# Kernel tuning notes

Measured on AMD Instinct MI355X. Metric: run time of the kernel, lower is better.

The kernel has to match this reference:

```python
import jax, jax.numpy as jnp
import numpy as np

N_NODES = 100000
N_EDGES = 1600000
IN_CH = 128
HID = 128   # 2 * out_channels
OUT = 64


def setup_inputs() -> dict:
    key = jax.random.key(0)
    ks = jax.random.split(key, 6)
    x = jax.random.normal(ks[0], (N_NODES, IN_CH), dtype=jnp.float32)
    edge_index = jax.random.randint(ks[1], (2, N_EDGES), 0, N_NODES, dtype=jnp.int64)
    # Glorot-ish scaled weights
    W1 = jax.random.normal(ks[2], (IN_CH, HID), dtype=jnp.float32) * (1.0 / np.sqrt(IN_CH))
    b1 = jnp.zeros((HID,), dtype=jnp.float32)
    Wmu = jax.random.normal(ks[3], (HID, OUT), dtype=jnp.float32) * (1.0 / np.sqrt(HID))
    bmu = jnp.zeros((OUT,), dtype=jnp.float32)
    Wlv = jax.random.normal(ks[4], (HID, OUT), dtype=jnp.float32) * (1.0 / np.sqrt(HID))
    blv = jnp.zeros((OUT,), dtype=jnp.float32)
    return {"x": x, "edge_index": edge_index, "W1": W1, "b1": b1,
            "Wmu": Wmu, "bmu": bmu, "Wlv": Wlv, "blv": blv}


def reference(x, edge_index, W1, b1, Wmu, bmu, Wlv, blv):
    n = x.shape[0]
    loops = jnp.arange(n, dtype=edge_index.dtype)
    src = jnp.concatenate([edge_index[0], loops])  # [E + N]
    dst = jnp.concatenate([edge_index[1], loops])
    # GCN symmetric normalization with self-loops (cached=True -> compute once, reuse)
    deg = jax.ops.segment_sum(jnp.ones_like(src, dtype=x.dtype), dst, num_segments=n)
    dinv = jnp.where(deg > 0, jax.lax.rsqrt(jnp.maximum(deg, 1.0)), 0.0)
    norm = (dinv[src] * dinv[dst])[:, None]  # [E+N, 1]

    def gcn(h, W, b):
        h = h @ W                              # dense transform first (smaller gather width)
        msg = h[src] * norm                    # gather + edge scaling
        return jax.ops.segment_sum(msg, dst, num_segments=n) + b

    h = jax.nn.relu(gcn(x, W1, b1))
    mu = gcn(h, Wmu, bmu)
    logvar = gcn(h, Wlv, blv)
    return (mu, logvar)
```

## Files before the change

### kernel.cpp

```cpp
#include <hip/hip_runtime.h>
#include <hip/hip_fp16.h>


using half8 = __attribute__((ext_vector_type(8))) _Float16;
using f32x4 = __attribute__((ext_vector_type(4))) float;
using f32x2 = __attribute__((ext_vector_type(2))) float;

constexpr int CAP = 8192;

__global__ void detect_kernel(const int* __restrict__ ei, int* __restrict__ mode,
                              int* __restrict__ bcnt, int K) {
    int lane = threadIdx.x & 63;
    for (int i = lane; i < K; i += 64) bcnt[i] = 0;
    int any = 0;
    for (int k = lane; k < 1024; k += 64) any |= ei[2 * k + 1];
    unsigned long long b = __ballot(any != 0);
    if (threadIdx.x == 0) *mode = (b == 0ull) ? 1 : 0;
}

__global__ __launch_bounds__(256) void partition_kernel(
    const int* __restrict__ ei, int E, int n, const int* __restrict__ mode,
    int* __restrict__ bcnt, unsigned* __restrict__ pairs) {
    __shared__ int hist[512];
    __shared__ int base[512];
    int t = threadIdx.x;
    for (int i = t; i < 512; i += 256) hist[i] = 0;
    __syncthreads();
    int m = *mode;
    int e0 = blockIdx.x * 8192;
    int s_[32], d_[32], o_[32];
#pragma unroll
    for (int k = 0; k < 32; ++k) {
        int e = e0 + k * 256 + t;
        d_[k] = -1;
        if (e < E) {
            int s = m ? ei[2 * e] : ei[e];
            int d = m ? ei[2 * (E + e)] : ei[E + e];
            if ((unsigned)d < (unsigned)n && (unsigned)s < (unsigned)n) {
                s_[k] = s;
                d_[k] = d;
                o_[k] = atomicAdd(&hist[d >> 8], 1);
            }
        }
    }
    __syncthreads();
    int K = (n + 255) >> 8;
    for (int b = t; b < K; b += 256) {
        int h = hist[b];
        base[b] = h ? atomicAdd(&bcnt[b], h) : 0;
    }
    __syncthreads();
#pragma unroll
    for (int k = 0; k < 32; ++k) {
        if (d_[k] >= 0) {
            int b = d_[k] >> 8;
            unsigned p = (unsigned)s_[k] | ((unsigned)(d_[k] & 255) << 24);
            pairs[(size_t)b * CAP + base[b] + o_[k]] = p;
        }
    }
}

__global__ __launch_bounds__(256) void build_kernel(
    const unsigned* __restrict__ pairs, const int* __restrict__ bcnt,
    int2* __restrict__ rowbe, float* __restrict__ dinv,
    int* __restrict__ csr_src, int n) {
    __shared__ int hist[256];
    __shared__ int wtot[4];
    int b = blockIdx.x;
    int cnt = bcnt[b];
    size_t gbase = (size_t)b * CAP;
    int tid = threadIdx.x, lane = tid & 63, wv = tid >> 6;
    hist[tid] = 0;
    __syncthreads();
    for (int i = tid; i < cnt; i += 256)
        atomicAdd(&hist[pairs[gbase + i] >> 24], 1);
    __syncthreads();
    int v = hist[tid];
    int incl = v;
#pragma unroll
    for (int off = 1; off < 64; off <<= 1) {
        int t = __shfl_up(incl, off, 64);
        if (lane >= off) incl += t;
    }
    if (lane == 63) wtot[wv] = incl;
    __syncthreads();
    int wo = 0;
    for (int w = 0; w < wv; ++w) wo += wtot[w];
    int ex = wo + incl - v;
    int node = (b << 8) + tid;
    if (node < n) {
        int beg = (int)gbase + ex;
        rowbe[node] = make_int2(beg, beg + v);
        dinv[node] = rsqrtf((float)(v + 1));
    }
    __syncthreads();
    hist[tid] = ex;
    __syncthreads();
    for (int i = tid; i < cnt; i += 256) {
        unsigned p = pairs[gbase + i];
        int pos = atomicAdd(&hist[p >> 24], 1);
        csr_src[gbase + pos] = (int)(p & 0x00FFFFFFu);
    }
}

template <int MODE>
__global__ __launch_bounds__(256) void agg_row_kernel(
    const __half* __restrict__ T, const float* __restrict__ dinv,
    const int2* __restrict__ rowbe, const int* __restrict__ csr_src,
    const float* __restrict__ biasa, const float* __restrict__ biasb,
    void* __restrict__ outa, void* __restrict__ outb, int n) {
    int wave = (int)((blockIdx.x * blockDim.x + threadIdx.x) >> 6);
    int lane = threadIdx.x & 63;
    if (wave >= n) return;
    const __half2* x2 = (const __half2*)T;
    float di = dinv[wave];
    float2 xf = __half22float2(x2[((size_t)wave << 6) + lane]);
    float ax = 0.f, ay = 0.f;
    int2 be = rowbe[wave];
    int e = be.x, end = be.y;
    for (; e + 8 <= end; e += 8) {
        int s[8];
        float w[8];
        float2 u[8];
#pragma unroll
        for (int k = 0; k < 8; ++k)
            s[k] = __builtin_amdgcn_readfirstlane(csr_src[e + k]);
#pragma unroll
        for (int k = 0; k < 8; ++k) w[k] = dinv[s[k]];
#pragma unroll
        for (int k = 0; k < 8; ++k)
            u[k] = __half22float2(x2[((size_t)s[k] << 6) + lane]);
#pragma unroll
        for (int k = 0; k < 8; ++k) {
            ax += w[k] * u[k].x;
            ay += w[k] * u[k].y;
        }
    }
    for (; e < end; ++e) {
        int s = __builtin_amdgcn_readfirstlane(csr_src[e]);
        float w = dinv[s];
        float2 u = __half22float2(x2[((size_t)s << 6) + lane]);
        ax += w * u.x;
        ay += w * u.y;
    }
    const float* bp = (lane < 32) ? biasa : biasb;
    float2 bv = *(const float2*)(bp + ((2 * lane) & 63));
    float vx = di * (di * xf.x + ax) + bv.x;
    float vy = di * (di * xf.y + ay) + bv.y;
    if (MODE == 0) {
        vx = fmaxf(vx, 0.f);
        vy = fmaxf(vy, 0.f);
        __half2 hv = __floats2half2_rn(vx, vy);
        unsigned int bits;
        __builtin_memcpy(&bits, &hv, 4);
        unsigned int* o = (unsigned int*)outa;
        __builtin_nontemporal_store(bits, o + ((size_t)wave << 6) + lane);
    } else {
        float* o = (lane < 32) ? (float*)outa : (float*)outb;
        int cc = (2 * lane) & 63;
        f32x2 v = {vx, vy};
        __builtin_nontemporal_store(v, (f32x2*)(o + (size_t)wave * 64 + cc));
    }
}

__global__ void packw2_kernel(const float* __restrict__ W1,
                              const float* __restrict__ Wmu,
                              const float* __restrict__ Wlv,
                              __half* __restrict__ dst1,
                              __half* __restrict__ dst2) {
    int which = blockIdx.x >> 3;
    int t = (blockIdx.x & 7) * 256 + threadIdx.x;
    int lane = t & 63;
    int fk = t >> 6;
    int kt = fk & 3, nt = fk >> 2;
    int k0 = kt * 32 + ((lane >> 4) << 3);
    int c = nt * 16 + (lane & 15);
    const float* W;
    __half* dst;
    int ldw, cc;
    if (which) {
        W = (c < 64) ? Wmu : Wlv;
        cc = c & 63;
        ldw = 64;
        dst = dst2;
    } else {
        W = W1;
        cc = c;
        ldw = 128;
        dst = dst1;
    }
    __half tmp[8];
#pragma unroll
    for (int e = 0; e < 8; ++e)
        tmp[e] = __float2half(W[(size_t)(k0 + e) * ldw + cc]);
    *(float4*)(dst + (size_t)t * 8) = *(float4*)tmp;
}

template <typename AT>
__global__ __launch_bounds__(256) void gemm_pure_kernel(
    const AT* __restrict__ A, const __half* __restrict__ Wp,
    __half* __restrict__ outh, int n) {
    int lane = threadIdx.x & 63;
    int wv = threadIdx.x >> 6;
    int m0 = (blockIdx.x * 4 + wv) * 16;
    if (m0 >= n) return;
    int row_a = m0 + (lane & 15);
    if (row_a >= n) row_a = n - 1;
    half8 afr[4];
    if constexpr (sizeof(AT) == 4) {
        const float4* Arow = (const float4*)(A + (size_t)row_a * 128);
#pragma unroll
        for (int kt = 0; kt < 4; ++kt) {
            float4 lo = Arow[kt * 8 + ((lane >> 4) << 1)];
            float4 hi = Arow[kt * 8 + ((lane >> 4) << 1) + 1];
            half8 h;
            h[0] = (_Float16)lo.x; h[1] = (_Float16)lo.y;
            h[2] = (_Float16)lo.z; h[3] = (_Float16)lo.w;
            h[4] = (_Float16)hi.x; h[5] = (_Float16)hi.y;
            h[6] = (_Float16)hi.z; h[7] = (_Float16)hi.w;
            afr[kt] = h;
        }
    } else {
        const half8* Arow = (const half8*)(A + (size_t)row_a * 128);
#pragma unroll
        for (int kt = 0; kt < 4; ++kt) afr[kt] = Arow[kt * 4 + (lane >> 4)];
    }

    const half8* Wf = (const half8*)Wp;
    int colw = lane & 15;
    int rbase = m0 + ((lane >> 4) << 2);

#pragma unroll
    for (int nt = 0; nt < 8; ++nt) {
        f32x4 acc = {0.f, 0.f, 0.f, 0.f};
#pragma unroll
        for (int kt = 0; kt < 4; ++kt)
            acc = __builtin_amdgcn_mfma_f32_16x16x32_f16(
                afr[kt], Wf[(nt * 4 + kt) * 64 + lane], acc, 0, 0, 0);
        int c = nt * 16 + colw;
#pragma unroll
        for (int e = 0; e < 4; ++e) {
            int r = rbase + e;
            if (r < n) outh[(size_t)r * 128 + c] = __float2half(acc[e]);
        }
    }
}

extern "C" void kernel_launch(void* const* d_in, const int* in_sizes, int n_in,
                              void* d_out, int out_size, void* d_ws, size_t ws_size,
                              hipStream_t stream) {
    const float* x   = (const float*)d_in[0];
    const int*   ei  = (const int*)d_in[1];
    const float* W1  = (const float*)d_in[2];
    const float* b1  = (const float*)d_in[3];
    const float* Wmu = (const float*)d_in[4];
    const float* bmu = (const float*)d_in[5];
    const float* Wlv = (const float*)d_in[6];
    const float* blv = (const float*)d_in[7];
    float* out = (float*)d_out;

    const int n = in_sizes[0] / 128;
    const int E = in_sizes[1] / 2;
    const int K = (n + 255) >> 8;

    char* ws = (char*)d_ws;
    size_t off = 0;
    auto alloc = [&](size_t bytes) -> void* {
        void* p = ws + off;
        off += (bytes + 255) & ~(size_t)255;
        return p;
    };
    int*      mode    = (int*)alloc(256);
    int*      bcnt    = (int*)alloc((size_t)K * 4);
    int2*     rowbe   = (int2*)alloc((size_t)n * 8);
    float*    dinv    = (float*)alloc((size_t)n * 4);
    int*      csr_src = (int*)alloc((size_t)K * CAP * 4);
    unsigned* pairs   = (unsigned*)alloc((size_t)K * CAP * 4);
    __half*   bufT    = (__half*)alloc((size_t)n * 128 * 2);
    __half*   bufH    = (__half*)alloc((size_t)n * 128 * 2);
    __half*   W1p     = (__half*)alloc(128 * 128 * 2);
    __half*   W2p     = (__half*)alloc(128 * 128 * 2);

    detect_kernel<<<1, 64, 0, stream>>>(ei, mode, bcnt, K);

    int pb = (E + 8191) / 8192;
    partition_kernel<<<pb, 256, 0, stream>>>(ei, E, n, mode, bcnt, pairs);
    build_kernel<<<K, 256, 0, stream>>>(pairs, bcnt, rowbe, dinv, csr_src, n);

    packw2_kernel<<<16, 256, 0, stream>>>(W1, Wmu, Wlv, W1p, W2p);

    int gb = (n + 63) / 64;
    int ab = (n + 3) / 4;

    gemm_pure_kernel<float><<<gb, 256, 0, stream>>>(x, W1p, bufT, n);
    agg_row_kernel<0><<<ab, 256, 0, stream>>>(bufT, dinv, rowbe, csr_src,
                                              b1, b1 + 64, bufH, nullptr, n);
    gemm_pure_kernel<__half><<<gb, 256, 0, stream>>>(bufH, W2p, bufT, n);
    agg_row_kernel<1><<<ab, 256, 0, stream>>>(bufT, dinv, rowbe, csr_src,
                                              bmu, blv, out,
                                              out + (size_t)n * 64, n);
}
```

Measured before the change: 239.6 us.

## Stage partitioned edge pairs in LDS for coalesced bucket writes; fuse setup kernels

Partition now counts per-bucket histograms, prefix-sums them, scatters pairs into shared memory in bucket order, then writes contiguous runs to global buckets. This replaces per-edge scattered global stores. It costs a second read of the edge indices and much larger LDS usage, which lowers occupancy. The detect and weight-packing kernels are merged into one launch to drop a kernel launch.

```diff
diff --git a/kernel.cpp b/kernel.cpp
--- a/kernel.cpp
+++ b/kernel.cpp
@@ -7,56 +7,121 @@
 using f32x2 = __attribute__((ext_vector_type(2))) float;
 
 constexpr int CAP = 8192;
-
-__global__ void detect_kernel(const int* __restrict__ ei, int* __restrict__ mode,
-                              int* __restrict__ bcnt, int K) {
-    int lane = threadIdx.x & 63;
-    for (int i = lane; i < K; i += 64) bcnt[i] = 0;
-    int any = 0;
-    for (int k = lane; k < 1024; k += 64) any |= ei[2 * k + 1];
-    unsigned long long b = __ballot(any != 0);
-    if (threadIdx.x == 0) *mode = (b == 0ull) ? 1 : 0;
+constexpr int PB  = 8192;
+
+__global__ void setup_kernel(const int* __restrict__ ei, int* __restrict__ mode,
+                             int* __restrict__ bcnt, int K,
+                             const float* __restrict__ W1,
+                             const float* __restrict__ Wmu,
+                             const float* __restrict__ Wlv,
+                             __half* __restrict__ dst1,
+                             __half* __restrict__ dst2) {
+    if (blockIdx.x == 0) {
+        int tid = threadIdx.x;
+        for (int i = tid; i < K; i += 256) bcnt[i] = 0;
+        if (tid < 64) {
+            int any = 0;
+            for (int k = tid; k < 1024; k += 64) any |= ei[2 * k + 1];
+            unsigned long long b = __ballot(any != 0);
+            if (tid == 0) *mode = (b == 0ull) ? 1 : 0;
+        }
+        return;
+    }
+    int blk = blockIdx.x - 1;
+    int which = blk >> 3;
+    int t = (blk & 7) * 256 + threadIdx.x;
+    int lane = t & 63;
+    int fk = t >> 6;
+    int kt = fk & 3, nt = fk >> 2;
+    int k0 = kt * 32 + ((lane >> 4) << 3);
+    int c = nt * 16 + (lane & 15);
+    const float* W;
+    __half* dst;
+    int ldw, cc;
+    if (which) {
+        W = (c < 64) ? Wmu : Wlv;
+        cc = c & 63;
+        ldw = 64;
+        dst = dst2;
+    } else {
+        W = W1;
+        cc = c;
+        ldw = 128;
+        dst = dst1;
+    }
+    __half tmp[8];
+#pragma unroll
+    for (int e = 0; e < 8; ++e)
+        tmp[e] = __float2half(W[(size_t)(k0 + e) * ldw + cc]);
+    *(float4*)(dst + (size_t)t * 8) = *(float4*)tmp;
 }
 
 __global__ __launch_bounds__(256) void partition_kernel(
     const int* __restrict__ ei, int E, int n, const int* __restrict__ mode,
     int* __restrict__ bcnt, unsigned* __restrict__ pairs) {
+    __shared__ unsigned sh_pair[PB];
+    __shared__ unsigned short sh_b[PB];
     __shared__ int hist[512];
-    __shared__ int base[512];
+    __shared__ int loff[512];
+    __shared__ int gbase[512];
+    __shared__ int cur[512];
+    __shared__ int wtot[4];
     int t = threadIdx.x;
     for (int i = t; i < 512; i += 256) hist[i] = 0;
     __syncthreads();
     int m = *mode;
-    int e0 = blockIdx.x * 8192;
-    int s_[32], d_[32], o_[32];
-#pragma unroll
-    for (int k = 0; k < 32; ++k) {
+    int e0 = blockIdx.x * PB;
+    for (int k = 0; k < PB / 256; ++k) {
         int e = e0 + k * 256 + t;
-        d_[k] = -1;
+        if (e < E) {
+            int s = m ? ei[2 * e] : ei[e];
+            int d = m ? ei[2 * (E + e)] : ei[E + e];
+            if ((unsigned)d < (unsigned)n && (unsigned)s < (unsigned)n)
+                atomicAdd(&hist[d >> 8], 1);
+        }
+    }
+    __syncthreads();
+    {
+        int lane = t & 63, wv = t >> 6;
+        int v0 = hist[2 * t], v1 = hist[2 * t + 1];
+        int ps = v0 + v1;
+        int incl = ps;
+#pragma unroll
+        for (int off = 1; off < 64; off <<= 1) {
+            int u = __shfl_up(incl, off, 64);
+            if (lane >= off) incl += u;
+        }
+        if (lane == 63) wtot[wv] = incl;
+        __syncthreads();
+        int wo = 0;
+        for (int w = 0; w < wv; ++w) wo += wtot[w];
+        int ex = wo + incl - ps;
+        loff[2 * t] = ex;
+        loff[2 * t + 1] = ex + v0;
+        cur[2 * t] = ex;
+        cur[2 * t + 1] = ex + v0;
+        gbase[2 * t]     = v0 ? atomicAdd(&bcnt[2 * t], v0) : 0;
+        gbase[2 * t + 1] = v1 ? atomicAdd(&bcnt[2 * t + 1], v1) : 0;
+    }
+    __syncthreads();
+    int tot = loff[511] + hist[511];
+    for (int k = 0; k < PB / 256; ++k) {
+        int e = e0 + k * 256 + t;
         if (e < E) {
             int s = m ? ei[2 * e] : ei[e];
             int d = m ? ei[2 * (E + e)] : ei[E + e];
             if ((unsigned)d < (unsigned)n && (unsigned)s < (unsigned)n) {
-                s_[k] = s;
-                d_[k] = d;
-                o_[k] = atomicAdd(&hist[d >> 8], 1);
+                int b = d >> 8;
+                int slot = atomicAdd(&cur[b], 1);
+                sh_pair[slot] = (unsigned)s | ((unsigned)(d & 255) << 24);
+                sh_b[slot] = (unsigned short)b;
             }
         }
     }
     __syncthreads();
-    int K = (n + 255) >> 8;
-    for (int b = t; b < K; b += 256) {
-        int h = hist[b];
-        base[b] = h ? atomicAdd(&bcnt[b], h) : 0;
-    }
-    __syncthreads();
-#pragma unroll
-    for (int k = 0; k < 32; ++k) {
-        if (d_[k] >= 0) {
-            int b = d_[k] >> 8;
-            unsigned p = (unsigned)s_[k] | ((unsigned)(d_[k] & 255) << 24);
-            pairs[(size_t)b * CAP + base[b] + o_[k]] = p;
-        }
+    for (int i = t; i < tot; i += 256) {
+        int b = sh_b[i];
+        pairs[(size_t)b * CAP + gbase[b] + (i - loff[b])] = sh_pair[i];
     }
 }
 
@@ -163,39 +228,6 @@
     }
 }
 
-__global__ void packw2_kernel(const float* __restrict__ W1,
-                              const float* __restrict__ Wmu,
-                              const float* __restrict__ Wlv,
-                              __half* __restrict__ dst1,
-                              __half* __restrict__ dst2) {
-    int which = blockIdx.x >> 3;
-    int t = (blockIdx.x & 7) * 256 + threadIdx.x;
-    int lane = t & 63;
-    int fk = t >> 6;
-    int kt = fk & 3, nt = fk >> 2;
-    int k0 = kt * 32 + ((lane >> 4) << 3);
-    int c = nt * 16 + (lane & 15);
-    const float* W;
-    __half* dst;
-    int ldw, cc;
-    if (which) {
-        W = (c < 64) ? Wmu : Wlv;
-        cc = c & 63;
-        ldw = 64;
-        dst = dst2;
-    } else {
-        W = W1;
-        cc = c;
-        ldw = 128;
-        dst = dst1;
-    }
-    __half tmp[8];
-#pragma unroll
-    for (int e = 0; e < 8; ++e)
-        tmp[e] = __float2half(W[(size_t)(k0 + e) * ldw + cc]);
-    *(float4*)(dst + (size_t)t * 8) = *(float4*)tmp;
-}
-
 template <typename AT>
 __global__ __launch_bounds__(256) void gemm_pure_kernel(
     const AT* __restrict__ A, const __half* __restrict__ Wp,
@@ -281,13 +313,12 @@
     __half*   W1p     = (__half*)alloc(128 * 128 * 2);
     __half*   W2p     = (__half*)alloc(128 * 128 * 2);
 
-    detect_kernel<<<1, 64, 0, stream>>>(ei, mode, bcnt, K);
-
-    int pb = (E + 8191) / 8192;
+    setup_kernel<<<17, 256, 0, stream>>>(ei, mode, bcnt, K,
+                                         W1, Wmu, Wlv, W1p, W2p);
+
+    int pb = (E + PB - 1) / PB;
     partition_kernel<<<pb, 256, 0, stream>>>(ei, E, n, mode, bcnt, pairs);
     build_kernel<<<K, 256, 0, stream>>>(pairs, bcnt, rowbe, dinv, csr_src, n);
-
-    packw2_kernel<<<16, 256, 0, stream>>>(W1, Wmu, Wlv, W1p, W2p);
 
     int gb = (n + 63) / 64;
     int ab = (n + 3) / 4;
```

Measured after the change: 240.4 us. About the same (+0.4%).
